# Performance work log

Hardware: AMD Instinct MI355X
Metric: run time of the kernel (lower is better)

Reference implementation:

```python
import jax, jax.numpy as jnp
import numpy as np

B, S, H, V = 256, 64, 512, 32000


def setup_inputs() -> dict:
    key = jax.random.key(0)
    ks = jax.random.split(key, 26)
    f32 = jnp.float32

    def n(k, shape, scale):
        return jax.random.normal(k, shape, dtype=f32) * scale

    s_h = 1.0 / np.sqrt(H)        # torch LSTMCell init scale ~ U(-1/sqrt(H),1/sqrt(H)); use normal of same scale
    s_2h = 1.0 / np.sqrt(2 * H)
    kn_h = np.sqrt(2.0 / H)       # kaiming_normal std for (B,H) tensor (fan_in = H)
    kn_2h = np.sqrt(2.0 / (2 * H))

    inp = {}
    inp["x"] = jax.random.randint(ks[0], (B, S), 0, V)
    inp["W_emb"] = n(ks[1], (V, H), 1.0)
    # forward cell
    inp["Wih_f"] = n(ks[2], (4 * H, H), s_h)
    inp["Whh_f"] = n(ks[3], (4 * H, H), s_h)
    inp["bih_f"] = n(ks[4], (4 * H,), s_h)
    inp["bhh_f"] = n(ks[5], (4 * H,), s_h)
    # backward cell
    inp["Wih_b"] = n(ks[6], (4 * H, H), s_h)
    inp["Whh_b"] = n(ks[7], (4 * H, H), s_h)
    inp["bih_b"] = n(ks[8], (4 * H,), s_h)
    inp["bhh_b"] = n(ks[9], (4 * H,), s_h)
    # combiner cell (input 2H, hidden 2H)
    inp["Wih_c"] = n(ks[10], (8 * H, 2 * H), s_2h)
    inp["Whh_c"] = n(ks[11], (8 * H, 2 * H), s_2h)
    inp["bih_c"] = n(ks[12], (8 * H,), s_2h)
    inp["bhh_c"] = n(ks[13], (8 * H,), s_2h)
    # linear head
    inp["Wout"] = n(ks[14], (V, 2 * H), s_2h)
    inp["bout"] = n(ks[15], (V,), s_2h)
    # kaiming-normal initial states
    inp["h0f"] = n(ks[16], (B, H), kn_h)
    inp["c0f"] = n(ks[17], (B, H), kn_h)
    inp["h0b"] = n(ks[18], (B, H), kn_h)
    inp["c0b"] = n(ks[19], (B, H), kn_h)
    inp["h0c"] = n(ks[20], (B, 2 * H), kn_2h)
    inp["c0c"] = n(ks[21], (B, 2 * H), kn_2h)
    return inp


def run_lstm(xs, h0, c0, Wih, Whh, b):
    # xs: (S, B, D). PyTorch LSTMCell gate order: i, f, g, o.
    def step(carry, x_t):
        h, c = carry
        g = x_t @ Wih.T + h @ Whh.T + b
        i, f, gg, o = jnp.split(g, 4, axis=-1)
        i = jax.nn.sigmoid(i)
        f = jax.nn.sigmoid(f)
        gg = jnp.tanh(gg)
        o = jax.nn.sigmoid(o)
        c2 = f * c + i * gg
        h2 = o * jnp.tanh(c2)
        return (h2, c2), h2
    _, hs = jax.lax.scan(step, (h0, c0), xs)
    return hs  # (S, B, hidden)


def reference(x, W_emb, Wih_f, Whh_f, bih_f, bhh_f, Wih_b, Whh_b, bih_b, bhh_b,
              Wih_c, Whh_c, bih_c, bhh_c, Wout, bout, h0f, c0f, h0b, c0b, h0c, c0c):
    b_sz, s_len = x.shape
    W = W_emb.at[0].set(0.0)                 # padding_idx=0
    emb = W[x]                               # (B, S, H)
    seq = emb.reshape(s_len, b_sz, -1)       # faithful to original .view(S, B, -1) (raw reshape, not transpose)
    hf = run_lstm(seq, h0f, c0f, Wih_f, Whh_f, bih_f + bhh_f)            # (S, B, H)
    hb = run_lstm(seq[::-1], h0b, c0b, Wih_b, Whh_b, bih_b + bhh_b)      # (S, B, H), produced order
    comb_in = jnp.concatenate([hf, hb], axis=-1)                          # (S, B, 2H)
    hc = run_lstm(comb_in, h0c, c0c, Wih_c, Whh_c, bih_c + bhh_c)        # (S, B, 2H)
    return hc[-1] @ Wout.T + bout                                         # (B, V)
```

## Files before the change

kernel.cpp:

```cpp
#include <hip/hip_runtime.h>

#define BB 256
#define SS 64
#define HH 512
#define VV 32000

typedef unsigned short u16;
typedef __attribute__((ext_vector_type(8))) short bf16x8;
typedef __attribute__((ext_vector_type(4))) float f32x4;

__device__ __forceinline__ float sigm(float x) { return 1.0f / (1.0f + __expf(-x)); }
__device__ __forceinline__ float tanh_fast(float x) { return 1.0f - 2.0f / (__expf(2.0f * x) + 1.0f); }
__device__ __forceinline__ u16 f2bf(float f) {
    unsigned u = __float_as_uint(f);
    return (u16)((u + 0x7fffu + ((u >> 16) & 1u)) >> 16);
}
__device__ __forceinline__ bf16x8 ld_cvt8(const float* s) {
    float4 v0 = *(const float4*)s, v1 = *(const float4*)(s + 4);
    bf16x8 b;
    b[0] = (short)f2bf(v0.x); b[1] = (short)f2bf(v0.y);
    b[2] = (short)f2bf(v0.z); b[3] = (short)f2bf(v0.w);
    b[4] = (short)f2bf(v1.x); b[5] = (short)f2bf(v1.y);
    b[6] = (short)f2bf(v1.z); b[7] = (short)f2bf(v1.w);
    return b;
}

#define MFMA(a, b, c) __builtin_amdgcn_mfma_f32_16x16x32_bf16(a, b, c, 0, 0, 0)

__global__ __launch_bounds__(256)
void pack_k(const int* __restrict__ x, const float* __restrict__ W_emb,
            const float* __restrict__ Wih_f, const float* __restrict__ Whh_f,
            const float* __restrict__ Wih_b, const float* __restrict__ Whh_b,
            const float* __restrict__ Wih_c, const float* __restrict__ Whh_c,
            u16* __restrict__ Xfrag, u16* __restrict__ Wfsw,
            u16* __restrict__ Wbsw, u16* __restrict__ Wcsw)
{
    const int lane = threadIdx.x & 63;
    const int l15 = lane & 15, quad = lane >> 4;
    const int gw0 = blockIdx.x * 4 + (threadIdx.x >> 6);
    const int nw = gridDim.x * 4;
    for (int task = gw0; task < 40960; task += nw) {
        const float* src; u16* dst; float scale = 1.f;
        if (task < 16384) {
            int s = task >> 8, rem = task & 255, mt = rem >> 4, kc = rem & 15;
            int b = mt * 16 + l15;
            int tok = x[s * 256 + b];
            scale = (tok == 0) ? 0.f : 1.f;
            src = W_emb + (size_t)tok * 512 + kc * 32 + quad * 8;
            dst = Xfrag + ((size_t)(s * 16 + mt) * 16 + kc) * 512 + (size_t)lane * 8;
        } else if (task < 24576) {
            int e = task - 16384;
            int which = e >> 12; e &= 4095;
            int ut = e >> 7, rem = e & 127, kc = rem >> 2, g = rem & 3;
            int row = g * 512 + ut * 16 + l15;
            int k0 = kc * 32 + quad * 8;
            const float* Wih = which ? Wih_b : Wih_f;
            const float* Whh = which ? Whh_b : Whh_f;
            src = (k0 < 512) ? (Wih + (size_t)row * 512 + k0)
                             : (Whh + (size_t)row * 512 + (k0 - 512));
            u16* W = which ? Wbsw : Wfsw;
            dst = W + ((size_t)(ut * 32 + kc) * 4 + g) * 512 + (size_t)lane * 8;
        } else {
            int e = task - 24576;
            int ut = e >> 8, rem = e & 255, kc = rem >> 2, g = rem & 3;
            int row = g * 1024 + ut * 16 + l15;
            int k0 = kc * 32 + quad * 8;
            src = (k0 < 1024) ? (Wih_c + (size_t)row * 1024 + k0)
                              : (Whh_c + (size_t)row * 1024 + (k0 - 1024));
            dst = Wcsw + ((size_t)(ut * 64 + kc) * 4 + g) * 512 + (size_t)lane * 8;
        }
        float4 v0 = *(const float4*)src;
        float4 v1 = *(const float4*)(src + 4);
        bf16x8 o;
        o[0] = (short)f2bf(v0.x * scale); o[1] = (short)f2bf(v0.y * scale);
        o[2] = (short)f2bf(v0.z * scale); o[3] = (short)f2bf(v0.w * scale);
        o[4] = (short)f2bf(v1.x * scale); o[5] = (short)f2bf(v1.y * scale);
        o[6] = (short)f2bf(v1.z * scale); o[7] = (short)f2bf(v1.w * scale);
        *(bf16x8*)dst = o;
    }
}

__global__ __launch_bounds__(256)
void init_k(const float* __restrict__ bih_f, const float* __restrict__ bhh_f,
            const float* __restrict__ bih_b, const float* __restrict__ bhh_b,
            const float* __restrict__ bih_c, const float* __restrict__ bhh_c,
            const float* __restrict__ h0f, const float* __restrict__ c0f,
            const float* __restrict__ h0b, const float* __restrict__ c0b,
            const float* __restrict__ h0c, const float* __restrict__ c0c,
            float* __restrict__ bsf, float* __restrict__ bsb, float* __restrict__ bsc,
            u16* __restrict__ hf0, u16* __restrict__ hb0, u16* __restrict__ hc0,
            float* __restrict__ cf, float* __restrict__ cb, float* __restrict__ cc)
{
    const int gid = blockIdx.x * 256 + threadIdx.x;
    if (gid < 2048)       bsf[gid] = bih_f[gid] + bhh_f[gid];
    else if (gid < 4096)  { int e = gid - 2048; bsb[e] = bih_b[e] + bhh_b[e]; }
    else if (gid < 8192)  { int e = gid - 4096; bsc[e] = bih_c[e] + bhh_c[e]; }
    const int stride = gridDim.x * 256;
    for (int i = gid; i < 131072; i += stride) {
        int b = i >> 9, k = i & 511;
        int dst = ((b >> 4) * 16 + (k >> 5)) * 512 + (((b & 15) + (((k >> 3) & 3) << 4)) << 3) + (k & 7);
        hf0[dst] = f2bf(h0f[i]);
        hb0[dst] = f2bf(h0b[i]);
        cf[i] = c0f[i];
        cb[i] = c0b[i];
    }
    for (int i = gid; i < 262144; i += stride) {
        int b = i >> 10, k = i & 1023;
        int dst = ((b >> 4) * 32 + (k >> 5)) * 512 + (((b & 15) + (((k >> 3) & 3) << 4)) << 3) + (k & 7);
        hc0[dst] = f2bf(h0c[i]);
        cc[i] = c0c[i];
    }
}

__global__ __launch_bounds__(256)
void step_k(const u16* __restrict__ Xfrag,
            const u16* __restrict__ Wfsw, const u16* __restrict__ Wbsw,
            const u16* __restrict__ Wcsw,
            const float* __restrict__ bsf, const float* __restrict__ bsb,
            const float* __restrict__ bsc,
            const u16* __restrict__ hf_r, u16* __restrict__ hf_w, float* __restrict__ cf,
            const u16* __restrict__ hb_r, u16* __restrict__ hb_w, float* __restrict__ cb,
            const u16* __restrict__ hc_r, u16* __restrict__ hc_w, float* __restrict__ cc,
            int t)
{
    __shared__ __align__(16) u16 Bsh[2][2][4][512];
    const int tid = threadIdx.x;
    const int w = tid >> 6, lane = tid & 63;
    const int l15 = lane & 15, quad = lane >> 4;
    const int xcd = blockIdx.x & 7, slot = blockIdx.x >> 3;
    const f32x4 z = {0.f, 0.f, 0.f, 0.f};

    if (slot < 16) {
        if (t >= SS) return;
        const int mh = slot & 1, cell = xcd >> 2;
        const int ut = (xcd & 3) * 8 + (slot >> 1);
        const int mt0 = mh * 8 + w * 2;
        const u16* Wsw = cell ? Wbsw : Wfsw;
        const float* bs = cell ? bsb : bsf;
        const u16* h_r = cell ? hb_r : hf_r;
        u16* h_w = cell ? hb_w : hf_w;
        float* c = cell ? cb : cf;
        const int s2 = cell ? (SS - 1 - t) : t;

        const u16* wstage = Wsw + (size_t)ut * 65536 + (size_t)w * 512 + (size_t)lane * 8;
        const u16* xb0 = Xfrag + ((size_t)(s2 * 16 + mt0) * 16) * 512 + (size_t)lane * 8;
        const u16* hp0 = h_r + ((size_t)(mt0 * 16)) * 512 + (size_t)lane * 8;

        f32x4 acc[2][4];
#pragma unroll
        for (int mi = 0; mi < 2; ++mi)
#pragma unroll
            for (int g = 0; g < 4; ++g) acc[mi][g] = z;

#define AFB(f) (((f) < 16) ? (xb0 + (size_t)(f) * 512) : (hp0 + (size_t)((f) - 16) * 512))
        bf16x8 aA0[3], aA1[3], aB0[3], aB1[3];
        {
            bf16x8 w00 = *(const bf16x8*)(wstage);
            bf16x8 w01 = *(const bf16x8*)(wstage + 2048);
            bf16x8 w10 = *(const bf16x8*)(wstage + 2 * 2048);
            bf16x8 w11 = *(const bf16x8*)(wstage + 3 * 2048);
            const u16* f0 = AFB(0);  const u16* f1 = AFB(1);
            const u16* f2 = AFB(2);  const u16* f3 = AFB(3);
            aA0[0] = *(const bf16x8*)f0; aA1[0] = *(const bf16x8*)(f0 + 8192);
            aB0[0] = *(const bf16x8*)f1; aB1[0] = *(const bf16x8*)(f1 + 8192);
            aA0[1] = *(const bf16x8*)f2; aA1[1] = *(const bf16x8*)(f2 + 8192);
            aB0[1] = *(const bf16x8*)f3; aB1[1] = *(const bf16x8*)(f3 + 8192);
            *(bf16x8*)&Bsh[0][0][w][(size_t)lane * 8] = w00;
            *(bf16x8*)&Bsh[0][1][w][(size_t)lane * 8] = w01;
            *(bf16x8*)&Bsh[1][0][w][(size_t)lane * 8] = w10;
            *(bf16x8*)&Bsh[1][1][w][(size_t)lane * 8] = w11;
            __syncthreads();
        }
#pragma unroll
        for (int p = 0; p < 16; ++p) {
            const int s = p % 3, sn = (p + 2) % 3, cur = p & 1;
            bf16x8 wr0, wr1;
            const bool pre = (p + 2 < 16);
            if (pre) {
                wr0 = *(const bf16x8*)(wstage + (size_t)(2 * p + 4) * 2048);
                wr1 = *(const bf16x8*)(wstage + (size_t)(2 * p + 5) * 2048);
                const u16* f0 = AFB(2 * p + 4);
                const u16* f1 = AFB(2 * p + 5);
                aA0[sn] = *(const bf16x8*)f0; aA1[sn] = *(const bf16x8*)(f0 + 8192);
                aB0[sn] = *(const bf16x8*)f1; aB1[sn] = *(const bf16x8*)(f1 + 8192);
            }
#pragma unroll
            for (int g = 0; g < 4; ++g) {
                bf16x8 b0 = *(const bf16x8*)&Bsh[cur][0][g][(size_t)lane * 8];
                bf16x8 b1 = *(const bf16x8*)&Bsh[cur][1][g][(size_t)lane * 8];
                acc[0][g] = MFMA(aA0[s], b0, acc[0][g]);
                acc[1][g] = MFMA(aA1[s], b0, acc[1][g]);
                acc[0][g] = MFMA(aB0[s], b1, acc[0][g]);
                acc[1][g] = MFMA(aB1[s], b1, acc[1][g]);
            }
            __syncthreads();
            if (pre) {
                *(bf16x8*)&Bsh[cur][0][w][(size_t)lane * 8] = wr0;
                *(bf16x8*)&Bsh[cur][1][w][(size_t)lane * 8] = wr1;
            }
        }
#undef AFB

        const int u = ut * 16 + l15;
        const float bi_ = bs[u], bf_ = bs[512 + u], bg_ = bs[1024 + u], bo_ = bs[1536 + u];
        const int fragk = ut >> 1;
        const int lanehi = ((ut & 1) * 2 + (l15 >> 3)) << 4;
        const int j = l15 & 7;
#pragma unroll
        for (int mi = 0; mi < 2; ++mi) {
            const int mt = mt0 + mi;
#pragma unroll
            for (int r = 0; r < 4; ++r) {
                const int b = mt * 16 + quad * 4 + r;
                const size_t ci = (size_t)b * 512 + u;
                float i_ = sigm(acc[mi][0][r] + bi_);
                float f_ = sigm(acc[mi][1][r] + bf_);
                float g_ = tanh_fast(acc[mi][2][r] + bg_);
                float o_ = sigm(acc[mi][3][r] + bo_);
                float c2 = f_ * c[ci] + i_ * g_;
                c[ci] = c2;
                h_w[(size_t)(mt * 16 + fragk) * 512 + (size_t)((quad * 4 + r) + lanehi) * 8 + j]
                    = f2bf(o_ * tanh_fast(c2));
            }
        }
    } else {
        if (t == 0) return;
        const int cs = slot - 16;
        const int mh = cs & 1;
        const int ut = xcd * 8 + (cs >> 1);
        const int mt0 = mh * 8 + w * 2;

        const u16* wstage = Wcsw + (size_t)ut * 131072 + (size_t)w * 512 + (size_t)lane * 8;
        const u16* hfa = hf_r + ((size_t)(mt0 * 16)) * 512 + (size_t)lane * 8;
        const u16* hba = hb_r + ((size_t)(mt0 * 16)) * 512 + (size_t)lane * 8;
        const u16* hca = hc_r + ((size_t)(mt0 * 32)) * 512 + (size_t)lane * 8;

        f32x4 acc[2][4];
#pragma unroll
        for (int mi = 0; mi < 2; ++mi)
#pragma unroll
            for (int g = 0; g < 4; ++g) acc[mi][g] = z;

#define ACB(f)  (((f) < 16) ? (hfa + (size_t)(f) * 512) \
               : ((f) < 32) ? (hba + (size_t)((f) - 16) * 512) \
                            : (hca + (size_t)((f) - 32) * 512))
#define ACB1(f) (((f) < 32) ? 8192 : 16384)
        bf16x8 aA0[3], aA1[3], aB0[3], aB1[3];
        {
            bf16x8 w00 = *(const bf16x8*)(wstage);
            bf16x8 w01 = *(const bf16x8*)(wstage + 2048);
            bf16x8 w10 = *(const bf16x8*)(wstage + 2 * 2048);
            bf16x8 w11 = *(const bf16x8*)(wstage + 3 * 2048);
            const u16* f0 = ACB(0);  const u16* f1 = ACB(1);
            const u16* f2 = ACB(2);  const u16* f3 = ACB(3);
            aA0[0] = *(const bf16x8*)f0; aA1[0] = *(const bf16x8*)(f0 + ACB1(0));
            aB0[0] = *(const bf16x8*)f1; aB1[0] = *(const bf16x8*)(f1 + ACB1(1));
            aA0[1] = *(const bf16x8*)f2; aA1[1] = *(const bf16x8*)(f2 + ACB1(2));
            aB0[1] = *(const bf16x8*)f3; aB1[1] = *(const bf16x8*)(f3 + ACB1(3));
            *(bf16x8*)&Bsh[0][0][w][(size_t)lane * 8] = w00;
            *(bf16x8*)&Bsh[0][1][w][(size_t)lane * 8] = w01;
            *(bf16x8*)&Bsh[1][0][w][(size_t)lane * 8] = w10;
            *(bf16x8*)&Bsh[1][1][w][(size_t)lane * 8] = w11;
            __syncthreads();
        }
#pragma unroll
        for (int p = 0; p < 32; ++p) {
            const int s = p % 3, sn = (p + 2) % 3, cur = p & 1;
            bf16x8 wr0, wr1;
            const bool pre = (p + 2 < 32);
            if (pre) {
                wr0 = *(const bf16x8*)(wstage + (size_t)(2 * p + 4) * 2048);
                wr1 = *(const bf16x8*)(wstage + (size_t)(2 * p + 5) * 2048);
                const u16* f0 = ACB(2 * p + 4);
                const u16* f1 = ACB(2 * p + 5);
                aA0[sn] = *(const bf16x8*)f0; aA1[sn] = *(const bf16x8*)(f0 + ACB1(2 * p + 4));
                aB0[sn] = *(const bf16x8*)f1; aB1[sn] = *(const bf16x8*)(f1 + ACB1(2 * p + 5));
            }
#pragma unroll
            for (int g = 0; g < 4; ++g) {
                bf16x8 b0 = *(const bf16x8*)&Bsh[cur][0][g][(size_t)lane * 8];
                bf16x8 b1 = *(const bf16x8*)&Bsh[cur][1][g][(size_t)lane * 8];
                acc[0][g] = MFMA(aA0[s], b0, acc[0][g]);
                acc[1][g] = MFMA(aA1[s], b0, acc[1][g]);
                acc[0][g] = MFMA(aB0[s], b1, acc[0][g]);
                acc[1][g] = MFMA(aB1[s], b1, acc[1][g]);
            }
            __syncthreads();
            if (pre) {
                *(bf16x8*)&Bsh[cur][0][w][(size_t)lane * 8] = wr0;
                *(bf16x8*)&Bsh[cur][1][w][(size_t)lane * 8] = wr1;
            }
        }
#undef ACB
#undef ACB1

        const int u = ut * 16 + l15;
        const float bi_ = bsc[u], bf_ = bsc[1024 + u], bg_ = bsc[2048 + u], bo_ = bsc[3072 + u];
        const int fragk = ut >> 1;
        const int lanehi = ((ut & 1) * 2 + (l15 >> 3)) << 4;
        const int j = l15 & 7;
#pragma unroll
        for (int mi = 0; mi < 2; ++mi) {
            const int mt = mt0 + mi;
#pragma unroll
            for (int r = 0; r < 4; ++r) {
                const int b = mt * 16 + quad * 4 + r;
                const size_t ci = (size_t)b * 1024 + u;
                float i_ = sigm(acc[mi][0][r] + bi_);
                float f_ = sigm(acc[mi][1][r] + bf_);
                float g_ = tanh_fast(acc[mi][2][r] + bg_);
                float o_ = sigm(acc[mi][3][r] + bo_);
                float c2 = f_ * cc[ci] + i_ * g_;
                cc[ci] = c2;
                hc_w[(size_t)(mt * 32 + fragk) * 512 + (size_t)((quad * 4 + r) + lanehi) * 8 + j]
                    = f2bf(o_ * tanh_fast(c2));
            }
        }
    }
}

__global__ __launch_bounds__(256)
void head_v3(const u16* __restrict__ A,
             const float* __restrict__ W,
             const float* __restrict__ bias,
             float* __restrict__ out)
{
    __shared__ __align__(16) u16 Bsh[2][2][4][512];
    const int tid = threadIdx.x;
    const int w = tid >> 6, lane = tid & 63;
    const int l15 = lane & 15, quad = lane >> 4;
    const int bid = blockIdx.x;
    const int ntw = bid * 4 + w;

    const float* wsrc = W + (size_t)(ntw * 16 + l15) * 1024 + (size_t)quad * 8;
    const u16* ha[4];
#pragma unroll
    for (int mi = 0; mi < 4; ++mi)
        ha[mi] = A + ((size_t)((w * 4 + mi) * 32)) * 512 + (size_t)lane * 8;

    f32x4 acc[4][4];
#pragma unroll
    for (int mi = 0; mi < 4; ++mi)
#pragma unroll
        for (int nt = 0; nt < 4; ++nt) acc[mi][nt] = {0.f, 0.f, 0.f, 0.f};

    {
        bf16x8 s0 = ld_cvt8(wsrc);
        bf16x8 s1 = ld_cvt8(wsrc + 32);
        *(bf16x8*)&Bsh[0][0][w][(size_t)lane * 8] = s0;
        *(bf16x8*)&Bsh[0][1][w][(size_t)lane * 8] = s1;
        __syncthreads();
    }
    for (int p = 0; p < 16; ++p) {
        const int cur = p & 1, nxt = cur ^ 1;
        bf16x8 sa, sb;
        const bool pre = (p + 1 < 16);
        if (pre) {
            sa = ld_cvt8(wsrc + (size_t)(2 * p + 2) * 32);
            sb = ld_cvt8(wsrc + (size_t)(2 * p + 3) * 32);
        }
        bf16x8 a0[4], a1[4];
#pragma unroll
        for (int mi = 0; mi < 4; ++mi) {
            a0[mi] = *(const bf16x8*)(ha[mi] + (size_t)(2 * p) * 512);
            a1[mi] = *(const bf16x8*)(ha[mi] + (size_t)(2 * p + 1) * 512);
        }
#pragma unroll
        for (int nt = 0; nt < 4; ++nt) {
            bf16x8 b0 = *(const bf16x8*)&Bsh[cur][0][nt][(size_t)lane * 8];
            bf16x8 b1 = *(const bf16x8*)&Bsh[cur][1][nt][(size_t)lane * 8];
#pragma unroll
            for (int mi = 0; mi < 4; ++mi) {
                acc[mi][nt] = MFMA(a0[mi], b0, acc[mi][nt]);
                acc[mi][nt] = MFMA(a1[mi], b1, acc[mi][nt]);
            }
        }
        if (pre) {
            *(bf16x8*)&Bsh[nxt][0][w][(size_t)lane * 8] = sa;
            *(bf16x8*)&Bsh[nxt][1][w][(size_t)lane * 8] = sb;
        }
        __syncthreads();
    }

#pragma unroll
    for (int nt = 0; nt < 4; ++nt) {
        const int n = (bid * 4 + nt) * 16 + l15;
        const float bv = bias[n];
#pragma unroll
        for (int mi = 0; mi < 4; ++mi) {
            const int mt = w * 4 + mi;
#pragma unroll
            for (int r = 0; r < 4; ++r)
                out[(size_t)(mt * 16 + quad * 4 + r) * VV + n] = acc[mi][nt][r] + bv;
        }
    }
}

extern "C" void kernel_launch(void* const* d_in, const int* in_sizes, int n_in,
                              void* d_out, int out_size, void* d_ws, size_t ws_size,
                              hipStream_t stream) {
    const int*   x     = (const int*)d_in[0];
    const float* W_emb = (const float*)d_in[1];
    const float* Wih_f = (const float*)d_in[2];
    const float* Whh_f = (const float*)d_in[3];
    const float* bih_f = (const float*)d_in[4];
    const float* bhh_f = (const float*)d_in[5];
    const float* Wih_b = (const float*)d_in[6];
    const float* Whh_b = (const float*)d_in[7];
    const float* bih_b = (const float*)d_in[8];
    const float* bhh_b = (const float*)d_in[9];
    const float* Wih_c = (const float*)d_in[10];
    const float* Whh_c = (const float*)d_in[11];
    const float* bih_c = (const float*)d_in[12];
    const float* bhh_c = (const float*)d_in[13];
    const float* Wout  = (const float*)d_in[14];
    const float* bout  = (const float*)d_in[15];
    const float* h0f   = (const float*)d_in[16];
    const float* c0f   = (const float*)d_in[17];
    const float* h0b   = (const float*)d_in[18];
    const float* c0b   = (const float*)d_in[19];
    const float* h0c   = (const float*)d_in[20];
    const float* c0c   = (const float*)d_in[21];

    char* p = (char*)d_ws;
    u16* Wfsw = (u16*)p; p += (size_t)2048 * 1024 * 2;
    u16* Wbsw = (u16*)p; p += (size_t)2048 * 1024 * 2;
    u16* Wcsw = (u16*)p; p += (size_t)4096 * 2048 * 2;
    u16* Xfrag = (u16*)p; p += (size_t)8388608 * 2;
    float* bsf = (float*)p; p += 2048 * 4;
    float* bsb = (float*)p; p += 2048 * 4;
    float* bsc = (float*)p; p += 4096 * 4;
    u16* hf[2]; hf[0] = (u16*)p; p += 131072 * 2; hf[1] = (u16*)p; p += 131072 * 2;
    u16* hb[2]; hb[0] = (u16*)p; p += 131072 * 2; hb[1] = (u16*)p; p += 131072 * 2;
    u16* hc[2]; hc[0] = (u16*)p; p += 262144 * 2; hc[1] = (u16*)p; p += 262144 * 2;
    float* cf = (float*)p; p += 131072 * 4;
    float* cb = (float*)p; p += 131072 * 4;
    float* cc = (float*)p; p += 262144 * 4;

    pack_k<<<dim3(2560), dim3(256), 0, stream>>>(
        x, W_emb, Wih_f, Whh_f, Wih_b, Whh_b, Wih_c, Whh_c,
        Xfrag, Wfsw, Wbsw, Wcsw);
    init_k<<<dim3(1024), dim3(256), 0, stream>>>(
        bih_f, bhh_f, bih_b, bhh_b, bih_c, bhh_c,
        h0f, c0f, h0b, c0b, h0c, c0c,
        bsf, bsb, bsc, hf[0], hb[0], hc[0], cf, cb, cc);

    for (int t = 0; t <= SS; ++t) {
        step_k<<<dim3(256), dim3(256), 0, stream>>>(
            Xfrag, Wfsw, Wbsw, Wcsw, bsf, bsb, bsc,
            hf[t & 1], hf[(t + 1) & 1], cf,
            hb[t & 1], hb[(t + 1) & 1], cb,
            hc[(t + 1) & 1], hc[t & 1], cc, t);
    }
    head_v3<<<dim3(500), dim3(256), 0, stream>>>(hc[0], Wout, bout, (float*)d_out);
}
```

Baseline: 1.462 ms.

## Split LSTM step work across twice as many blocks, one M-tile per wave

Each step kernel block now covers a quarter of the batch rows instead of half, with each wave handling a single 16-row M tile rather than two. The grid doubles from 256 to 512 blocks so more CUs work on the latency-bound recurrent step, and each wave needs fewer accumulators and A-fragment registers. In exchange, each weight tile staged through shared memory is reused across fewer rows, so total weight traffic from L2 doubles.

```diff
diff --git a/kernel.cpp b/kernel.cpp
--- a/kernel.cpp
+++ b/kernel.cpp
@@ -130,11 +130,12 @@
     const int xcd = blockIdx.x & 7, slot = blockIdx.x >> 3;
     const f32x4 z = {0.f, 0.f, 0.f, 0.f};
 
-    if (slot < 16) {
+    if (slot < 32) {
         if (t >= SS) return;
-        const int mh = slot & 1, cell = xcd >> 2;
-        const int ut = (xcd & 3) * 8 + (slot >> 1);
-        const int mt0 = mh * 8 + w * 2;
+        const int cell = xcd >> 2;
+        const int ut = (xcd & 3) * 8 + (slot >> 2);
+        const int mq = slot & 3;
+        const int mt = mq * 4 + w;
         const u16* Wsw = cell ? Wbsw : Wfsw;
         const float* bs = cell ? bsb : bsf;
         const u16* h_r = cell ? hb_r : hf_r;
@@ -143,28 +144,22 @@
         const int s2 = cell ? (SS - 1 - t) : t;
 
         const u16* wstage = Wsw + (size_t)ut * 65536 + (size_t)w * 512 + (size_t)lane * 8;
-        const u16* xb0 = Xfrag + ((size_t)(s2 * 16 + mt0) * 16) * 512 + (size_t)lane * 8;
-        const u16* hp0 = h_r + ((size_t)(mt0 * 16)) * 512 + (size_t)lane * 8;
-
-        f32x4 acc[2][4];
-#pragma unroll
-        for (int mi = 0; mi < 2; ++mi)
-#pragma unroll
-            for (int g = 0; g < 4; ++g) acc[mi][g] = z;
+        const u16* xb0 = Xfrag + ((size_t)(s2 * 16 + mt) * 16) * 512 + (size_t)lane * 8;
+        const u16* hp0 = h_r + ((size_t)(mt * 16)) * 512 + (size_t)lane * 8;
+
+        f32x4 acc[4];
+#pragma unroll
+        for (int g = 0; g < 4; ++g) acc[g] = z;
 
 #define AFB(f) (((f) < 16) ? (xb0 + (size_t)(f) * 512) : (hp0 + (size_t)((f) - 16) * 512))
-        bf16x8 aA0[3], aA1[3], aB0[3], aB1[3];
+        bf16x8 a0[3], a1[3];
         {
             bf16x8 w00 = *(const bf16x8*)(wstage);
             bf16x8 w01 = *(const bf16x8*)(wstage + 2048);
             bf16x8 w10 = *(const bf16x8*)(wstage + 2 * 2048);
             bf16x8 w11 = *(const bf16x8*)(wstage + 3 * 2048);
-            const u16* f0 = AFB(0);  const u16* f1 = AFB(1);
-            const u16* f2 = AFB(2);  const u16* f3 = AFB(3);
-            aA0[0] = *(const bf16x8*)f0; aA1[0] = *(const bf16x8*)(f0 + 8192);
-            aB0[0] = *(const bf16x8*)f1; aB1[0] = *(const bf16x8*)(f1 + 8192);
-            aA0[1] = *(const bf16x8*)f2; aA1[1] = *(const bf16x8*)(f2 + 8192);
-            aB0[1] = *(const bf16x8*)f3; aB1[1] = *(const bf16x8*)(f3 + 8192);
+            a0[0] = *(const bf16x8*)AFB(0); a1[0] = *(const bf16x8*)AFB(1);
+            a0[1] = *(const bf16x8*)AFB(2); a1[1] = *(const bf16x8*)AFB(3);
             *(bf16x8*)&Bsh[0][0][w][(size_t)lane * 8] = w00;
             *(bf16x8*)&Bsh[0][1][w][(size_t)lane * 8] = w01;
             *(bf16x8*)&Bsh[1][0][w][(size_t)lane * 8] = w10;
@@ -179,19 +174,15 @@
             if (pre) {
                 wr0 = *(const bf16x8*)(wstage + (size_t)(2 * p + 4) * 2048);
                 wr1 = *(const bf16x8*)(wstage + (size_t)(2 * p + 5) * 2048);
-                const u16* f0 = AFB(2 * p + 4);
-                const u16* f1 = AFB(2 * p + 5);
-                aA0[sn] = *(const bf16x8*)f0; aA1[sn] = *(const bf16x8*)(f0 + 8192);
-                aB0[sn] = *(const bf16x8*)f1; aB1[sn] = *(const bf16x8*)(f1 + 8192);
+                a0[sn] = *(const bf16x8*)AFB(2 * p + 4);
+                a1[sn] = *(const bf16x8*)AFB(2 * p + 5);
             }
 #pragma unroll
             for (int g = 0; g < 4; ++g) {
                 bf16x8 b0 = *(const bf16x8*)&Bsh[cur][0][g][(size_t)lane * 8];
                 bf16x8 b1 = *(const bf16x8*)&Bsh[cur][1][g][(size_t)lane * 8];
-                acc[0][g] = MFMA(aA0[s], b0, acc[0][g]);
-                acc[1][g] = MFMA(aA1[s], b0, acc[1][g]);
-                acc[0][g] = MFMA(aB0[s], b1, acc[0][g]);
-                acc[1][g] = MFMA(aB1[s], b1, acc[1][g]);
+                acc[g] = MFMA(a0[s], b0, acc[g]);
+                acc[g] = MFMA(a1[s], b1, acc[g]);
             }
             __syncthreads();
             if (pre) {
@@ -207,56 +198,45 @@
         const int lanehi = ((ut & 1) * 2 + (l15 >> 3)) << 4;
         const int j = l15 & 7;
 #pragma unroll
-        for (int mi = 0; mi < 2; ++mi) {
-            const int mt = mt0 + mi;
-#pragma unroll
-            for (int r = 0; r < 4; ++r) {
-                const int b = mt * 16 + quad * 4 + r;
-                const size_t ci = (size_t)b * 512 + u;
-                float i_ = sigm(acc[mi][0][r] + bi_);
-                float f_ = sigm(acc[mi][1][r] + bf_);
-                float g_ = tanh_fast(acc[mi][2][r] + bg_);
-                float o_ = sigm(acc[mi][3][r] + bo_);
-                float c2 = f_ * c[ci] + i_ * g_;
-                c[ci] = c2;
-                h_w[(size_t)(mt * 16 + fragk) * 512 + (size_t)((quad * 4 + r) + lanehi) * 8 + j]
-                    = f2bf(o_ * tanh_fast(c2));
-            }
+        for (int r = 0; r < 4; ++r) {
+            const int b = mt * 16 + quad * 4 + r;
+            const size_t ci = (size_t)b * 512 + u;
+            float i_ = sigm(acc[0][r] + bi_);
+            float f_ = sigm(acc[1][r] + bf_);
+            float g_ = tanh_fast(acc[2][r] + bg_);
+            float o_ = sigm(acc[3][r] + bo_);
+            float c2 = f_ * c[ci] + i_ * g_;
+            c[ci] = c2;
+            h_w[(size_t)(mt * 16 + fragk) * 512 + (size_t)((quad * 4 + r) + lanehi) * 8 + j]
+                = f2bf(o_ * tanh_fast(c2));
         }
     } else {
         if (t == 0) return;
-        const int cs = slot - 16;
-        const int mh = cs & 1;
-        const int ut = xcd * 8 + (cs >> 1);
-        const int mt0 = mh * 8 + w * 2;
+        const int cs = slot - 32;
+        const int ut = xcd * 8 + (cs >> 2);
+        const int mq = cs & 3;
+        const int mt = mq * 4 + w;
 
         const u16* wstage = Wcsw + (size_t)ut * 131072 + (size_t)w * 512 + (size_t)lane * 8;
-        const u16* hfa = hf_r + ((size_t)(mt0 * 16)) * 512 + (size_t)lane * 8;
-        const u16* hba = hb_r + ((size_t)(mt0 * 16)) * 512 + (size_t)lane * 8;
-        const u16* hca = hc_r + ((size_t)(mt0 * 32)) * 512 + (size_t)lane * 8;
-
-        f32x4 acc[2][4];
-#pragma unroll
-        for (int mi = 0; mi < 2; ++mi)
-#pragma unroll
-            for (int g = 0; g < 4; ++g) acc[mi][g] = z;
+        const u16* hfa = hf_r + ((size_t)(mt * 16)) * 512 + (size_t)lane * 8;
+        const u16* hba = hb_r + ((size_t)(mt * 16)) * 512 + (size_t)lane * 8;
+        const u16* hca = hc_r + ((size_t)(mt * 32)) * 512 + (size_t)lane * 8;
+
+        f32x4 acc[4];
+#pragma unroll
+        for (int g = 0; g < 4; ++g) acc[g] = z;
 
 #define ACB(f)  (((f) < 16) ? (hfa + (size_t)(f) * 512) \
                : ((f) < 32) ? (hba + (size_t)((f) - 16) * 512) \
                             : (hca + (size_t)((f) - 32) * 512))
-#define ACB1(f) (((f) < 32) ? 8192 : 16384)
-        bf16x8 aA0[3], aA1[3], aB0[3], aB1[3];
+        bf16x8 a0[3], a1[3];
         {
             bf16x8 w00 = *(const bf16x8*)(wstage);
             bf16x8 w01 = *(const bf16x8*)(wstage + 2048);
             bf16x8 w10 = *(const bf16x8*)(wstage + 2 * 2048);
             bf16x8 w11 = *(const bf16x8*)(wstage + 3 * 2048);
-            const u16* f0 = ACB(0);  const u16* f1 = ACB(1);
-            const u16* f2 = ACB(2);  const u16* f3 = ACB(3);
-            aA0[0] = *(const bf16x8*)f0; aA1[0] = *(const bf16x8*)(f0 + ACB1(0));
-            aB0[0] = *(const bf16x8*)f1; aB1[0] = *(const bf16x8*)(f1 + ACB1(1));
-            aA0[1] = *(const bf16x8*)f2; aA1[1] = *(const bf16x8*)(f2 + ACB1(2));
-            aB0[1] = *(const bf16x8*)f3; aB1[1] = *(const bf16x8*)(f3 + ACB1(3));
+            a0[0] = *(const bf16x8*)ACB(0); a1[0] = *(const bf16x8*)ACB(1);
+            a0[1] = *(const bf16x8*)ACB(2); a1[1] = *(const bf16x8*)ACB(3);
             *(bf16x8*)&Bsh[0][0][w][(size_t)lane * 8] = w00;
             *(bf16x8*)&Bsh[0][1][w][(size_t)lane * 8] = w01;
             *(bf16x8*)&Bsh[1][0][w][(size_t)lane * 8] = w10;
@@ -271,19 +251,15 @@
             if (pre) {
                 wr0 = *(const bf16x8*)(wstage + (size_t)(2 * p + 4) * 2048);
                 wr1 = *(const bf16x8*)(wstage + (size_t)(2 * p + 5) * 2048);
-                const u16* f0 = ACB(2 * p + 4);
-                const u16* f1 = ACB(2 * p + 5);
-                aA0[sn] = *(const bf16x8*)f0; aA1[sn] = *(const bf16x8*)(f0 + ACB1(2 * p + 4));
-                aB0[sn] = *(const bf16x8*)f1; aB1[sn] = *(const bf16x8*)(f1 + ACB1(2 * p + 5));
+                a0[sn] = *(const bf16x8*)ACB(2 * p + 4);
+                a1[sn] = *(const bf16x8*)ACB(2 * p + 5);
             }
 #pragma unroll
             for (int g = 0; g < 4; ++g) {
                 bf16x8 b0 = *(const bf16x8*)&Bsh[cur][0][g][(size_t)lane * 8];
                 bf16x8 b1 = *(const bf16x8*)&Bsh[cur][1][g][(size_t)lane * 8];
-                acc[0][g] = MFMA(aA0[s], b0, acc[0][g]);
-                acc[1][g] = MFMA(aA1[s], b0, acc[1][g]);
-                acc[0][g] = MFMA(aB0[s], b1, acc[0][g]);
-                acc[1][g] = MFMA(aB1[s], b1, acc[1][g]);
+                acc[g] = MFMA(a0[s], b0, acc[g]);
+                acc[g] = MFMA(a1[s], b1, acc[g]);
             }
             __syncthreads();
             if (pre) {
@@ -292,7 +268,6 @@
             }
         }
 #undef ACB
-#undef ACB1
 
         const int u = ut * 16 + l15;
         const float bi_ = bsc[u], bf_ = bsc[1024 + u], bg_ = bsc[2048 + u], bo_ = bsc[3072 + u];
@@ -300,21 +275,17 @@
         const int lanehi = ((ut & 1) * 2 + (l15 >> 3)) << 4;
         const int j = l15 & 7;
 #pragma unroll
-        for (int mi = 0; mi < 2; ++mi) {
-            const int mt = mt0 + mi;
-#pragma unroll
-            for (int r = 0; r < 4; ++r) {
-                const int b = mt * 16 + quad * 4 + r;
-                const size_t ci = (size_t)b * 1024 + u;
-                float i_ = sigm(acc[mi][0][r] + bi_);
-                float f_ = sigm(acc[mi][1][r] + bf_);
-                float g_ = tanh_fast(acc[mi][2][r] + bg_);
-                float o_ = sigm(acc[mi][3][r] + bo_);
-                float c2 = f_ * cc[ci] + i_ * g_;
-                cc[ci] = c2;
-                hc_w[(size_t)(mt * 32 + fragk) * 512 + (size_t)((quad * 4 + r) + lanehi) * 8 + j]
-                    = f2bf(o_ * tanh_fast(c2));
-            }
+        for (int r = 0; r < 4; ++r) {
+            const int b = mt * 16 + quad * 4 + r;
+            const size_t ci = (size_t)b * 1024 + u;
+            float i_ = sigm(acc[0][r] + bi_);
+            float f_ = sigm(acc[1][r] + bf_);
+            float g_ = tanh_fast(acc[2][r] + bg_);
+            float o_ = sigm(acc[3][r] + bo_);
+            float c2 = f_ * cc[ci] + i_ * g_;
+            cc[ci] = c2;
+            hc_w[(size_t)(mt * 32 + fragk) * 512 + (size_t)((quad * 4 + r) + lanehi) * 8 + j]
+                = f2bf(o_ * tanh_fast(c2));
         }
     }
 }
@@ -446,7 +417,7 @@
         bsf, bsb, bsc, hf[0], hb[0], hc[0], cf, cb, cc);
 
     for (int t = 0; t <= SS; ++t) {
-        step_k<<<dim3(256), dim3(256), 0, stream>>>(
+        step_k<<<dim3(512), dim3(256), 0, stream>>>(
             Xfrag, Wfsw, Wbsw, Wcsw, bsf, bsb, bsc,
             hf[t & 1], hf[(t + 1) & 1], cf,
             hb[t & 1], hb[(t + 1) & 1], cb,
```

After: 1.185 ms. 1.23x faster.
